# Performance work log

Measured on AMD Instinct MI355X. Metric: run time of the kernel, lower is better.

Reference implementation:

```python
import jax, jax.numpy as jnp
import numpy as np

N, DIM, H = 4096, 768, 12
HD = DIM // H  # head_dim = 64


def setup_inputs() -> dict:
    key = jax.random.key(0)
    ks = jax.random.split(key, 7)
    std = 1.0 / np.sqrt(HD)
    return {
        "seq": jax.random.normal(ks[0], (N, DIM), dtype=jnp.float32),
        "Wq": jax.random.normal(ks[1], (H, HD, HD), dtype=jnp.float32) * std,
        "bq": jax.random.normal(ks[2], (H, HD), dtype=jnp.float32) * std,
        "Wk": jax.random.normal(ks[3], (H, HD, HD), dtype=jnp.float32) * std,
        "bk": jax.random.normal(ks[4], (H, HD), dtype=jnp.float32) * std,
        "Wv": jax.random.normal(ks[5], (H, HD, HD), dtype=jnp.float32) * std,
        "bv": jax.random.normal(ks[6], (H, HD), dtype=jnp.float32) * std,
    }


def reference(seq, Wq, bq, Wk, bk, Wv, bv):
    n = seq.shape[0]
    # split the feature dim into heads: [N, H, HD]
    s = seq.reshape(n, H, HD)
    # per-head linear projections (torch Linear: y = x W^T + b; W stored as [in,out])
    q = jnp.einsum("nhd,hde->hne", s, Wq) + bq[:, None, :]  # [H, N, HD]
    k = jnp.einsum("nhd,hde->hne", s, Wk) + bk[:, None, :]
    v = jnp.einsum("nhd,hde->hne", s, Wv) + bv[:, None, :]
    scale = 1.0 / jnp.sqrt(jnp.asarray(HD, dtype=seq.dtype))
    scores = jnp.einsum("hne,hme->hnm", q, k) * scale  # [H, N, N]
    attn = jax.nn.softmax(scores, axis=-1)
    out = jnp.einsum("hnm,hme->hne", attn, v)  # [H, N, HD]
    # hstack of per-head results == concat along features in head order
    return jnp.transpose(out, (1, 0, 2)).reshape(n, DIM)
```

## Files before the change

kernel.cpp:

```cpp
#include <hip/hip_runtime.h>
#include <stdint.h>
#include <stddef.h>

#define N   4096
#define DIM 768
#define H   12
#define HD  64

typedef __attribute__((ext_vector_type(4))) int   i32x4;
typedef __attribute__((ext_vector_type(4))) float f32x4;
typedef __attribute__((ext_vector_type(8))) short short8;

#define MFMA(acc, a, b) \
  acc = __builtin_amdgcn_mfma_f32_16x16x32_bf16(a, b, acc, 0, 0, 0)

#define GLOAD_LDS(gsrc, ldst) \
  __builtin_amdgcn_global_load_lds( \
      (const __attribute__((address_space(1))) uint32_t*)(gsrc), \
      (__attribute__((address_space(3))) uint32_t*)(ldst), 16, 0, 0)

static __device__ __forceinline__ float fast_exp2(float x) {
#if __has_builtin(__builtin_amdgcn_exp2f)
  return __builtin_amdgcn_exp2f(x);
#else
  return exp2f(x);
#endif
}

static __device__ __forceinline__ int pack_bf16(float lo, float hi) {
  const uint32_t ulo = __builtin_bit_cast(uint32_t, lo) + 0x8000u;
  const uint32_t uhi = __builtin_bit_cast(uint32_t, hi) + 0x8000u;
  return (int)__builtin_amdgcn_perm(uhi, ulo, 0x07060302u);
}

static __device__ __forceinline__ short to_bf16(float x) {
  union { float f; uint32_t u; } v; v.f = x;
  uint32_t u = v.u;
  u += 0x7fffu + ((u >> 16) & 1u);
  return (short)(u >> 16);
}

__global__ __launch_bounds__(256) void proj_kernel(
    const float* __restrict__ seq,
    const float* __restrict__ Wq, const float* __restrict__ bq,
    const float* __restrict__ Wk, const float* __restrict__ bk,
    const float* __restrict__ Wv, const float* __restrict__ bv,
    short* __restrict__ Qo, short* __restrict__ Ko, short* __restrict__ Vto)
{
  __shared__ float sT[64][68];
  __shared__ float w_lds[3][64][64];
  const int h  = blockIdx.y;
  const int r0 = blockIdx.x * 64;
  const int t  = (int)threadIdx.x;

#pragma unroll
  for (int i = 0; i < 16; ++i) {
    const int idx = t + i * 256;
    const int r = idx >> 6, c = idx & 63;
    sT[c][r]       = seq[(size_t)(r0 + r) * DIM + h * HD + c];
    w_lds[0][r][c] = Wq[h * 4096 + idx];
    w_lds[1][r][c] = Wk[h * 4096 + idx];
    w_lds[2][r][c] = Wv[h * 4096 + idx];
  }
  __syncthreads();

  const int w = t >> 6, l = t & 63;
  const int rb = w * 16;
  float aq[16], ak[16], av[16];
  const float bqv = bq[h * HD + l];
  const float bkv = bk[h * HD + l];
  const float bvv = bv[h * HD + l];
#pragma unroll
  for (int r = 0; r < 16; ++r) { aq[r] = bqv; ak[r] = bkv; av[r] = bvv; }

#pragma unroll 4
  for (int d = 0; d < 64; ++d) {
    const float wq = w_lds[0][d][l];
    const float wk = w_lds[1][d][l];
    const float wv = w_lds[2][d][l];
    const f32x4* sp = (const f32x4*)&sT[d][rb];
    const f32x4 s0 = sp[0], s1 = sp[1], s2 = sp[2], s3 = sp[3];
#pragma unroll
    for (int r = 0; r < 4; ++r) {
      aq[r]      = fmaf(s0[r], wq, aq[r]);
      ak[r]      = fmaf(s0[r], wk, ak[r]);
      av[r]      = fmaf(s0[r], wv, av[r]);
      aq[4 + r]  = fmaf(s1[r], wq, aq[4 + r]);
      ak[4 + r]  = fmaf(s1[r], wk, ak[4 + r]);
      av[4 + r]  = fmaf(s1[r], wv, av[4 + r]);
      aq[8 + r]  = fmaf(s2[r], wq, aq[8 + r]);
      ak[8 + r]  = fmaf(s2[r], wk, ak[8 + r]);
      av[8 + r]  = fmaf(s2[r], wv, av[8 + r]);
      aq[12 + r] = fmaf(s3[r], wq, aq[12 + r]);
      ak[12 + r] = fmaf(s3[r], wk, ak[12 + r]);
      av[12 + r] = fmaf(s3[r], wv, av[12 + r]);
    }
  }

  const float QSC = 0.1803368801111204f;
#pragma unroll
  for (int r = 0; r < 16; ++r) {
    const int n = r0 + rb + r;
    Qo[((size_t)h * N + n) * HD + l] = to_bf16(aq[r] * QSC);
    Ko[((size_t)h * N + n) * HD + l] = to_bf16(ak[r]);
    const int loc = n & 63;
    const int ns  = (n & ~63) | ((loc & 0x1C) << 1) | ((loc & 32) >> 3) | (loc & 3);
    Vto[((size_t)h * HD + l) * N + ns] = to_bf16(av[r]);
  }
}

__global__ __launch_bounds__(256) void attn_kernel(
    const short* __restrict__ Q, const short* __restrict__ K,
    const short* __restrict__ Vt, float* __restrict__ out)
{
  __shared__ __align__(16) char lds[32768];

  const int h  = blockIdx.y;
  const int q0 = blockIdx.x * 64;
  const int t  = (int)threadIdx.x;
  const int w  = t >> 6, l = t & 63, lr = l & 15, lg = l >> 4;

  const short* __restrict__ Qw = Q + ((size_t)h * N + q0 + w * 16) * HD;
  const char*  __restrict__ Kb = (const char*)(K  + (size_t)h * N * HD);
  const char*  __restrict__ Vb = (const char*)(Vt + (size_t)h * HD * N);

  short8 qf[2];
#pragma unroll
  for (int ds = 0; ds < 2; ++ds)
    qf[ds] = *(const short8*)(Qw + lr * HD + ds * 32 + lg * 8);

  f32x4 o[4], o5;
  o5 = f32x4{0.f, 0.f, 0.f, 0.f};
#pragma unroll
  for (int eb = 0; eb < 4; ++eb) o[eb] = f32x4{0.f, 0.f, 0.f, 0.f};
  const short8 vones = {0x3F80, 0x3F80, 0x3F80, 0x3F80,
                        0x3F80, 0x3F80, 0x3F80, 0x3F80};

  const int c0   = w * 2;
  const int c1   = c0 + 1;
  const int sr0  = c0 * 8 + (l >> 3);
  const int sr1  = sr0 + 8;
  const int scol = ((l & 7) * 16) ^ ((l >> 3) << 4);
  const int kdo0 = c0 * 1024 + l * 16;
  const int kdo1 = c1 * 1024 + l * 16;
  const char* const ks0 = Kb + (size_t)sr0 * 128 + scol;
  const char* const ks1 = Kb + (size_t)sr1 * 128 + scol;
  const char* const vs0 = Vb + (size_t)sr0 * (N * 2) + scol;
  const char* const vs1 = Vb + (size_t)sr1 * (N * 2) + scol;

  GLOAD_LDS(ks0, lds + kdo0);
  GLOAD_LDS(ks1, lds + kdo1);
  GLOAD_LDS(vs0, lds + 8192 + kdo0);
  GLOAD_LDS(vs1, lds + 8192 + kdo1);
  __syncthreads();

  for (int it = 0; it < N / 64; ++it) {
    const int  j1 = (it + 1) * 64;
    const bool pf = j1 < N;
    if (pf) {
      char* const nb = lds + ((it + 1) & 1) * 16384;
      GLOAD_LDS(ks0 + (size_t)j1 * 128, nb + kdo0);
      GLOAD_LDS(ks1 + (size_t)j1 * 128, nb + kdo1);
      GLOAD_LDS(vs0 + (size_t)j1 * 2,   nb + 8192 + kdo0);
      GLOAD_LDS(vs1 + (size_t)j1 * 2,   nb + 8192 + kdo1);
    }
    const char* k_lds = lds + (it & 1) * 16384;
    const char* v_lds = k_lds + 8192;

    f32x4 s[4];
#pragma unroll
    for (int kb = 0; kb < 4; ++kb) {
      const int krow = kb * 16 + lr;
      const int kswz = (krow & 7) << 4;
      const char* kr = k_lds + krow * 128;
      const short8 kf0 = *(const short8*)(kr + ((lg * 16) ^ kswz));
      const short8 kf1 = *(const short8*)(kr + ((64 + lg * 16) ^ kswz));
      f32x4 acc = {0.f, 0.f, 0.f, 0.f};
      MFMA(acc, kf0, qf[0]);
      MFMA(acc, kf1, qf[1]);
      s[kb] = acc;
    }

#pragma unroll
    for (int kb = 0; kb < 4; ++kb)
#pragma unroll
      for (int r = 0; r < 4; ++r)
        s[kb][r] = fast_exp2(s[kb][r]);

    i32x4 p0, p1;
    p0[0] = pack_bf16(s[0][0], s[0][1]);
    p0[1] = pack_bf16(s[0][2], s[0][3]);
    p0[2] = pack_bf16(s[2][0], s[2][1]);
    p0[3] = pack_bf16(s[2][2], s[2][3]);
    p1[0] = pack_bf16(s[1][0], s[1][1]);
    p1[1] = pack_bf16(s[1][2], s[1][3]);
    p1[2] = pack_bf16(s[3][0], s[3][1]);
    p1[3] = pack_bf16(s[3][2], s[3][3]);
    const short8 pa0 = __builtin_bit_cast(short8, p0);
    const short8 pa1 = __builtin_bit_cast(short8, p1);

    MFMA(o5, pa0, vones);
    MFMA(o5, pa1, vones);
#pragma unroll
    for (int eb = 0; eb < 4; ++eb) {
      const int vrow = eb * 16 + lr;
      const int vswz = (vrow & 7) << 4;
      const char* vr = v_lds + vrow * 128;
      const short8 vf0 = *(const short8*)(vr + ((lg * 16) ^ vswz));
      const short8 vf1 = *(const short8*)(vr + ((64 + lg * 16) ^ vswz));
      MFMA(o[eb], pa0, vf0);
      MFMA(o[eb], pa1, vf1);
    }

    __syncthreads();
  }

#pragma unroll
  for (int r = 0; r < 4; ++r) {
    const float inv = 1.0f / o5[r];
    const int n = q0 + w * 16 + lg * 4 + r;
    float* orow = out + (size_t)n * DIM + h * HD;
#pragma unroll
    for (int eb = 0; eb < 4; ++eb)
      orow[eb * 16 + lr] = o[eb][r] * inv;
  }
}

extern "C" void kernel_launch(void* const* d_in, const int* in_sizes, int n_in,
                              void* d_out, int out_size, void* d_ws, size_t ws_size,
                              hipStream_t stream) {
  const float* seq = (const float*)d_in[0];
  const float* Wq  = (const float*)d_in[1];
  const float* bq  = (const float*)d_in[2];
  const float* Wk  = (const float*)d_in[3];
  const float* bk  = (const float*)d_in[4];
  const float* Wv  = (const float*)d_in[5];
  const float* bv  = (const float*)d_in[6];
  float* out = (float*)d_out;

  short* Qw  = (short*)d_ws;
  short* Kw  = Qw + (size_t)H * N * HD;
  short* Vtw = Kw + (size_t)H * N * HD;

  proj_kernel<<<dim3(N / 64, H), 256, 0, stream>>>(seq, Wq, bq, Wk, bk, Wv, bv,
                                                   Qw, Kw, Vtw);
  attn_kernel<<<dim3(N / 64, H), 256, 0, stream>>>(Qw, Kw, Vtw, out);
}
```

Measured before the change: 108.3 us.

## Split attention KV range across two blocks and add a combine kernel

The attention grid gains a z dimension of 2, so each block processes half of the key/value tiles. Each half writes its unnormalized partial output and its row sum to workspace, and a new combine kernel adds the two halves and divides by the summed row sums. The aim is more blocks in flight and better latency hiding, at the cost of extra global traffic for the partial outputs and one more kernel launch. Separately, the projection kernel now reads the weights straight from global memory instead of staging them in LDS, which saves shared memory and a staging pass.

```diff
diff --git a/kernel.cpp b/kernel.cpp
--- a/kernel.cpp
+++ b/kernel.cpp
@@ -48,7 +48,6 @@
     short* __restrict__ Qo, short* __restrict__ Ko, short* __restrict__ Vto)
 {
   __shared__ float sT[64][68];
-  __shared__ float w_lds[3][64][64];
   const int h  = blockIdx.y;
   const int r0 = blockIdx.x * 64;
   const int t  = (int)threadIdx.x;
@@ -57,10 +56,7 @@
   for (int i = 0; i < 16; ++i) {
     const int idx = t + i * 256;
     const int r = idx >> 6, c = idx & 63;
-    sT[c][r]       = seq[(size_t)(r0 + r) * DIM + h * HD + c];
-    w_lds[0][r][c] = Wq[h * 4096 + idx];
-    w_lds[1][r][c] = Wk[h * 4096 + idx];
-    w_lds[2][r][c] = Wv[h * 4096 + idx];
+    sT[c][r] = seq[(size_t)(r0 + r) * DIM + h * HD + c];
   }
   __syncthreads();
 
@@ -73,11 +69,15 @@
 #pragma unroll
   for (int r = 0; r < 16; ++r) { aq[r] = bqv; ak[r] = bkv; av[r] = bvv; }
 
+  const float* __restrict__ Wqb = Wq + h * 4096;
+  const float* __restrict__ Wkb = Wk + h * 4096;
+  const float* __restrict__ Wvb = Wv + h * 4096;
+
 #pragma unroll 4
   for (int d = 0; d < 64; ++d) {
-    const float wq = w_lds[0][d][l];
-    const float wk = w_lds[1][d][l];
-    const float wv = w_lds[2][d][l];
+    const float wq = Wqb[d * 64 + l];
+    const float wk = Wkb[d * 64 + l];
+    const float wv = Wvb[d * 64 + l];
     const f32x4* sp = (const f32x4*)&sT[d][rb];
     const f32x4 s0 = sp[0], s1 = sp[1], s2 = sp[2], s3 = sp[3];
 #pragma unroll
@@ -111,14 +111,20 @@
 
 __global__ __launch_bounds__(256) void attn_kernel(
     const short* __restrict__ Q, const short* __restrict__ K,
-    const short* __restrict__ Vt, float* __restrict__ out)
+    const short* __restrict__ Vt, float* __restrict__ out,
+    float* __restrict__ oB, float* __restrict__ o5a, float* __restrict__ o5b)
 {
   __shared__ __align__(16) char lds[32768];
 
   const int h  = blockIdx.y;
   const int q0 = blockIdx.x * 64;
+  const int z  = blockIdx.z;
   const int t  = (int)threadIdx.x;
   const int w  = t >> 6, l = t & 63, lr = l & 15, lg = l >> 4;
+
+  const int ntile = (N / 64) / gridDim.z;
+  const int it0   = z * ntile;
+  const int itE   = it0 + ntile;
 
   const short* __restrict__ Qw = Q + ((size_t)h * N + q0 + w * 16) * HD;
   const char*  __restrict__ Kb = (const char*)(K  + (size_t)h * N * HD);
@@ -148,21 +154,23 @@
   const char* const vs0 = Vb + (size_t)sr0 * (N * 2) + scol;
   const char* const vs1 = Vb + (size_t)sr1 * (N * 2) + scol;
 
-  GLOAD_LDS(ks0, lds + kdo0);
-  GLOAD_LDS(ks1, lds + kdo1);
-  GLOAD_LDS(vs0, lds + 8192 + kdo0);
-  GLOAD_LDS(vs1, lds + 8192 + kdo1);
+  {
+    char* const b0 = lds + (it0 & 1) * 16384;
+    GLOAD_LDS(ks0 + (size_t)it0 * 8192, b0 + kdo0);
+    GLOAD_LDS(ks1 + (size_t)it0 * 8192, b0 + kdo1);
+    GLOAD_LDS(vs0 + (size_t)it0 * 128,  b0 + 8192 + kdo0);
+    GLOAD_LDS(vs1 + (size_t)it0 * 128,  b0 + 8192 + kdo1);
+  }
   __syncthreads();
 
-  for (int it = 0; it < N / 64; ++it) {
-    const int  j1 = (it + 1) * 64;
-    const bool pf = j1 < N;
+  for (int it = it0; it < itE; ++it) {
+    const bool pf = (it + 1) < itE;
     if (pf) {
       char* const nb = lds + ((it + 1) & 1) * 16384;
-      GLOAD_LDS(ks0 + (size_t)j1 * 128, nb + kdo0);
-      GLOAD_LDS(ks1 + (size_t)j1 * 128, nb + kdo1);
-      GLOAD_LDS(vs0 + (size_t)j1 * 2,   nb + 8192 + kdo0);
-      GLOAD_LDS(vs1 + (size_t)j1 * 2,   nb + 8192 + kdo1);
+      GLOAD_LDS(ks0 + (size_t)(it + 1) * 8192, nb + kdo0);
+      GLOAD_LDS(ks1 + (size_t)(it + 1) * 8192, nb + kdo1);
+      GLOAD_LDS(vs0 + (size_t)(it + 1) * 128,  nb + 8192 + kdo0);
+      GLOAD_LDS(vs1 + (size_t)(it + 1) * 128,  nb + 8192 + kdo1);
     }
     const char* k_lds = lds + (it & 1) * 16384;
     const char* v_lds = k_lds + 8192;
@@ -215,15 +223,48 @@
     __syncthreads();
   }
 
-#pragma unroll
-  for (int r = 0; r < 4; ++r) {
-    const float inv = 1.0f / o5[r];
-    const int n = q0 + w * 16 + lg * 4 + r;
-    float* orow = out + (size_t)n * DIM + h * HD;
-#pragma unroll
-    for (int eb = 0; eb < 4; ++eb)
-      orow[eb * 16 + lr] = o[eb][r] * inv;
-  }
+  if (gridDim.z == 1) {
+#pragma unroll
+    for (int r = 0; r < 4; ++r) {
+      const float inv = 1.0f / o5[r];
+      const int n = q0 + w * 16 + lg * 4 + r;
+      float* orow = out + (size_t)n * DIM + h * HD;
+#pragma unroll
+      for (int eb = 0; eb < 4; ++eb)
+        orow[eb * 16 + lr] = o[eb][r] * inv;
+    }
+  } else {
+    float* dsto = (z == 0) ? out : oB;
+    float* dst5 = (z == 0) ? o5a : o5b;
+#pragma unroll
+    for (int r = 0; r < 4; ++r) {
+      const int n = q0 + w * 16 + lg * 4 + r;
+      float* orow = dsto + (size_t)n * DIM + h * HD;
+#pragma unroll
+      for (int eb = 0; eb < 4; ++eb)
+        orow[eb * 16 + lr] = o[eb][r];
+      dst5[(size_t)h * N + n] = o5[r];
+    }
+  }
+}
+
+__global__ __launch_bounds__(256) void combine_kernel(
+    float* __restrict__ out, const float* __restrict__ oB,
+    const float* __restrict__ o5a, const float* __restrict__ o5b)
+{
+  const int i4   = blockIdx.x * 256 + (int)threadIdx.x;
+  const int base = i4 * 4;
+  const int n    = base / DIM;
+  const int c    = base - n * DIM;
+  const int hh   = c >> 6;
+  const size_t di = (size_t)hh * N + n;
+  const float inv = 1.0f / (o5a[di] + o5b[di]);
+  const f32x4 a = *(const f32x4*)(out + base);
+  const f32x4 b = *(const f32x4*)(oB + base);
+  f32x4 r;
+#pragma unroll
+  for (int j = 0; j < 4; ++j) r[j] = (a[j] + b[j]) * inv;
+  *(f32x4*)(out + base) = r;
 }
 
 extern "C" void kernel_launch(void* const* d_in, const int* in_sizes, int n_in,
@@ -238,11 +279,26 @@
   const float* bv  = (const float*)d_in[6];
   float* out = (float*)d_out;
 
+  const size_t qkv = (size_t)H * N * HD;
   short* Qw  = (short*)d_ws;
-  short* Kw  = Qw + (size_t)H * N * HD;
-  short* Vtw = Kw + (size_t)H * N * HD;
+  short* Kw  = Qw + qkv;
+  short* Vtw = Kw + qkv;
+  float* oB  = (float*)(Vtw + qkv);
+  float* o5a = oB + (size_t)N * DIM;
+  float* o5b = o5a + (size_t)H * N;
+
+  const size_t needed = 3 * qkv * sizeof(short)
+                      + ((size_t)N * DIM + 2 * (size_t)H * N) * sizeof(float);
+  const bool split = ws_size >= needed;
 
   proj_kernel<<<dim3(N / 64, H), 256, 0, stream>>>(seq, Wq, bq, Wk, bk, Wv, bv,
                                                    Qw, Kw, Vtw);
-  attn_kernel<<<dim3(N / 64, H), 256, 0, stream>>>(Qw, Kw, Vtw, out);
-}
+  if (split) {
+    attn_kernel<<<dim3(N / 64, H, 2), 256, 0, stream>>>(Qw, Kw, Vtw, out,
+                                                        oB, o5a, o5b);
+    combine_kernel<<<dim3(N * DIM / 1024), 256, 0, stream>>>(out, oB, o5a, o5b);
+  } else {
+    attn_kernel<<<dim3(N / 64, H, 1), 256, 0, stream>>>(Qw, Kw, Vtw, out,
+                                                        oB, o5a, o5b);
+  }
+}
```

Measured after the change: 113.3 us. +4.6%, slower.
